# Kernel optimization log

Hardware: AMD Instinct MI355X
Metric: run time of the kernel (lower is better)

## Reference

```python
import jax, jax.numpy as jnp
import numpy as np

B, L, DIM, H = 2, 2048, 1024, 16
HD = DIM // H  # head dim = 64
MASK_SCALE = -10 * 6  # faithful to the original source: mask_expand *= -10 * 6


def setup_inputs() -> dict:
    key = jax.random.key(0)
    ks = jax.random.split(key, 8)
    s = 1.0 / np.sqrt(DIM)
    return {
        "x": jax.random.normal(ks[0], (B, L, DIM), jnp.float32),
        "attention_mask": jax.random.uniform(ks[1], (B, L, L), jnp.float32),
        "Wq": jax.random.normal(ks[2], (DIM, DIM), jnp.float32) * s,
        "bq": jnp.zeros((DIM,), jnp.float32),
        "Wk": jax.random.normal(ks[3], (DIM, DIM), jnp.float32) * s,
        "bk": jnp.zeros((DIM,), jnp.float32),
        "Wv": jax.random.normal(ks[4], (DIM, DIM), jnp.float32) * s,
        "bv": jnp.zeros((DIM,), jnp.float32),
    }


def _split_heads(t):
    # [B, L, DIM] -> [B, H, L, HD]
    return t.reshape(B, L, H, HD).transpose(0, 2, 1, 3)


def reference(x, attention_mask, Wq, bq, Wk, bk, Wv, bv):
    q = _split_heads(x @ Wq + bq)
    k = _split_heads(x @ Wk + bk)
    v = _split_heads(x @ Wv + bv)
    scale = float(HD) ** -0.5
    # full [B, H, L, L] score matrix, as in the original
    scores = jnp.einsum("bhqd,bhkd->bhqk", q, k) * scale
    scores = scores + attention_mask[:, None, :, :] * MASK_SCALE
    probs = jax.nn.softmax(scores, axis=-1)
    ctx = jnp.einsum("bhqk,bhkd->bhqd", probs, v)
    # merge heads back: [B, L, DIM]
    return ctx.transpose(0, 2, 1, 3).reshape(B, L, DIM)
```

## Files before the change

### kernel.cpp

```cpp
#include <hip/hip_runtime.h>

#define LL 2048
#define NHEADS 16
#define HDIM 64
#define QSCALE 0.18033688011112042f
#define MASKC1 -86.56170245333780f

typedef __attribute__((ext_vector_type(8))) __bf16 bf16x8;
typedef __attribute__((ext_vector_type(4))) float f32x4;
typedef __attribute__((ext_vector_type(16))) float f32x16;
typedef __attribute__((ext_vector_type(4))) int i32x4;

__device__ __forceinline__ unsigned short f2bf(float f) {
  unsigned int u = __builtin_bit_cast(unsigned int, f);
  u += 0x7fffu + ((u >> 16) & 1u);
  return (unsigned short)(u >> 16);
}

__device__ __forceinline__ bf16x8 ld_frag(const unsigned short* p) {
  return *reinterpret_cast<const bf16x8*>(p);
}

__device__ __forceinline__ void async_cp16(const unsigned short* g, unsigned short* l) {
  __builtin_amdgcn_global_load_lds(
      (const __attribute__((address_space(1))) unsigned int*)(unsigned long long)(g),
      (__attribute__((address_space(3))) unsigned int*)(unsigned int)(unsigned long long)(l),
      16, 0, 0);
}

__global__ __launch_bounds__(256) void prep_kernel(
    const float* __restrict__ x, const float* __restrict__ Wq, const float* __restrict__ Wk,
    const float* __restrict__ Wv, unsigned short* __restrict__ xb,
    unsigned short* __restrict__ WtAll) {
  __shared__ float t[64][65];
  int blk = blockIdx.x;
  if (blk < 4096) {
    int i = (blk * 256 + threadIdx.x) * 4;
    float4 v = *reinterpret_cast<const float4*>(x + i);
    ushort4 o;
    o.x = f2bf(v.x); o.y = f2bf(v.y); o.z = f2bf(v.z); o.w = f2bf(v.w);
    *reinterpret_cast<ushort4*>(xb + i) = o;
  } else {
    int idx = blk - 4096;
    int z = idx >> 8; idx &= 255;
    const float* W = (z == 0) ? Wq : (z == 1) ? Wk : Wv;
    unsigned short* dst = WtAll + (size_t)z * 1024 * 1024;
    int n0 = (idx & 15) * 64, k0 = (idx >> 4) * 64;
    int tx = threadIdx.x & 63, ty = threadIdx.x >> 6;
#pragma unroll
    for (int p = 0; p < 16; ++p) {
      int kr = p * 4 + ty;
      t[kr][tx] = W[(size_t)(k0 + kr) * 1024 + n0 + tx];
    }
    __syncthreads();
#pragma unroll
    for (int p = 0; p < 16; ++p) {
      int nr = p * 4 + ty;
      dst[(size_t)(n0 + nr) * 1024 + k0 + tx] = f2bf(t[tx][nr]);
    }
  }
}

__global__ __launch_bounds__(256) void em_prep_kernel(const float* __restrict__ mask,
                                                      unsigned short* __restrict__ em) {
  unsigned int t = blockIdx.x * 256 + threadIdx.x;
  int p = t & 15;
  int q = (t >> 4) & 2047;
  int kb = (t >> 15) & 31;
  int b = t >> 20;
  const float* src = mask + ((size_t)b * LL + q) * LL + kb * 64;
  ushort4 o;
  o.x = f2bf(__builtin_amdgcn_exp2f(src[2 * p]      * MASKC1));
  o.y = f2bf(__builtin_amdgcn_exp2f(src[32 + 2 * p] * MASKC1));
  o.z = f2bf(__builtin_amdgcn_exp2f(src[2 * p + 1]  * MASKC1));
  o.w = f2bf(__builtin_amdgcn_exp2f(src[33 + 2 * p] * MASKC1));
  *reinterpret_cast<ushort4*>(em + (((size_t)b * 32 + kb) * LL + q) * 64 + 4 * p) = o;
}

__global__ __launch_bounds__(256) void qkv_gemm_kernel(
    const unsigned short* __restrict__ xb, const unsigned short* __restrict__ WtAll,
    const float* __restrict__ bq, const float* __restrict__ bk, const float* __restrict__ bv,
    unsigned short* __restrict__ qkv) {
  const int z = blockIdx.z;
  const unsigned short* Wt = WtAll + (size_t)z * 1024 * 1024;
  const float* bias = (z == 0) ? bq : (z == 1) ? bk : bv;
  unsigned short* outb = qkv + (size_t)z * 4194304;

  __shared__ __align__(16) unsigned short smem[16384];
  unsigned short* As = smem;
  unsigned short* Bs = smem + 8192;

  const int tid = threadIdx.x;
  const int w = tid >> 6, lane = tid & 63, g = lane >> 4, cc = lane & 15;
  const int wm = w >> 1, wn = w & 1;
  const int m0 = blockIdx.y * 128, n0 = blockIdx.x * 128;
  const int srow = lane >> 3;
  const int gc = ((lane & 7) - srow) & 7;
  const unsigned short* ga = xb + (size_t)(m0 + w * 32 + srow) * 1024 + gc * 8;
  const unsigned short* gb = Wt + (size_t)(n0 + w * 32 + srow) * 1024 + gc * 8;
  unsigned short* la = As + w * 2048;
  unsigned short* lb = Bs + w * 2048;

  f32x4 acc[4][4];
#pragma unroll
  for (int i = 0; i < 4; ++i)
#pragma unroll
    for (int j = 0; j < 4; ++j) acc[i][j] = (f32x4)0.0f;

  for (int kk = 0; kk < 1024; kk += 64) {
    __syncthreads();
#pragma unroll
    for (int i = 0; i < 4; ++i) {
      async_cp16(ga + i * 8192 + kk, la + i * 512);
      async_cp16(gb + i * 8192 + kk, lb + i * 512);
    }
    __syncthreads();
    bf16x8 af[4][2], bfr[4][2];
#pragma unroll
    for (int mt = 0; mt < 4; ++mt)
#pragma unroll
      for (int ks = 0; ks < 2; ++ks)
        af[mt][ks] = ld_frag(&As[(wm * 64 + mt * 16 + cc) * 64 + ((4 * ks + g + cc) & 7) * 8]);
#pragma unroll
    for (int nt = 0; nt < 4; ++nt)
#pragma unroll
      for (int ks = 0; ks < 2; ++ks)
        bfr[nt][ks] = ld_frag(&Bs[(wn * 64 + nt * 16 + cc) * 64 + ((4 * ks + g + cc) & 7) * 8]);
#pragma unroll
    for (int mt = 0; mt < 4; ++mt)
#pragma unroll
      for (int nt = 0; nt < 4; ++nt)
#pragma unroll
        for (int ks = 0; ks < 2; ++ks)
          acc[mt][nt] = __builtin_amdgcn_mfma_f32_16x16x32_bf16(af[mt][ks], bfr[nt][ks],
                                                                acc[mt][nt], 0, 0, 0);
  }

  if (z != 2) {
    const float sc = (z == 0) ? QSCALE : 1.0f;
#pragma unroll
    for (int nt = 0; nt < 4; ++nt) {
      int n = n0 + wn * 64 + nt * 16 + cc;
      float bval = bias[n];
      int h = n >> 6, d = n & 63;
#pragma unroll
      for (int mt = 0; mt < 4; ++mt) {
#pragma unroll
        for (int r = 0; r < 4; ++r) {
          int m = m0 + wm * 64 + mt * 16 + g * 4 + r;
          int b = m >> 11, l = m & 2047;
          outb[(((size_t)(b * NHEADS + h) * LL) + l) * HDIM + d] =
              f2bf((acc[mt][nt][r] + bval) * sc);
        }
      }
    }
  } else {
    __syncthreads();
#pragma unroll
    for (int nt = 0; nt < 4; ++nt) {
      int nr = wn * 64 + nt * 16 + cc;
      float bval = bias[n0 + nr];
#pragma unroll
      for (int mt = 0; mt < 4; ++mt)
#pragma unroll
        for (int r = 0; r < 4; ++r)
          smem[nr * 128 + wm * 64 + 32 * (mt & 1) + 8 * g + 2 * r + (mt >> 1)] =
              f2bf(acc[mt][nt][r] + bval);
    }
    __syncthreads();
    int row = tid >> 1, half = tid & 1;
    int n = n0 + row, hh = n >> 6, dd = n & 63;
    int bb = m0 >> 11;
    int tI = ((m0 & 2047) >> 6) + half;
    unsigned short* dst =
        outb + (size_t)(bb * NHEADS + hh) * (LL * HDIM) + (size_t)tI * 4096 + dd * 64;
#pragma unroll
    for (int i = 0; i < 8; ++i)
      *reinterpret_cast<uint4*>(dst + i * 8) =
          *reinterpret_cast<const uint4*>(&smem[row * 128 + half * 64 + i * 8]);
  }
}

__global__ __launch_bounds__(128, 2) void flash_kernel(
    const unsigned short* __restrict__ Qb, const unsigned short* __restrict__ Kb,
    const unsigned short* __restrict__ Vt, const unsigned short* __restrict__ Em,
    float* __restrict__ out) {
  const int bh = blockIdx.y, b = bh >> 4, h = bh & 15;
  const int q0 = blockIdx.x * 64;
  const int tid = threadIdx.x, w = tid >> 6, lane = tid & 63;
  const int cl = lane & 31, hf = lane >> 5;
  const size_t bhoff = (size_t)bh * (LL * HDIM);

  __shared__ __align__(16) unsigned short Ks[2][64 * 64];
  __shared__ __align__(16) unsigned short Vs[2][64 * 64];
  __shared__ __align__(16) unsigned short Ps[2][32 * 64];
  unsigned short* myP = Ps[w];

  bf16x8 aq[4];
  {
    const unsigned short* qp = Qb + bhoff + (size_t)(q0 + w * 32 + cl) * HDIM + hf * 8;
#pragma unroll
    for (int ks = 0; ks < 4; ++ks) aq[ks] = ld_frag(qp + ks * 16);
  }

  const int srow = lane >> 3;
  const int gcs = ((lane & 7) - srow) & 7;
  const unsigned short* kgp = Kb + bhoff + (size_t)(w * 32 + srow) * 64 + gcs * 8;
  const unsigned short* vgp = Vt + bhoff + (size_t)(w * 32 + srow) * 64 + gcs * 8;

  i32x4 onesi = {0x3F803F80, 0x3F803F80, 0x3F803F80, 0x3F803F80};
  bf16x8 vones = __builtin_bit_cast(bf16x8, onesi);

  f32x16 oacc0 = (f32x16)0.0f, oacc1 = (f32x16)0.0f, liacc = (f32x16)0.0f;

  const unsigned short* ebase =
      Em + (((size_t)b * 32) * LL + (q0 + w * 32 + 4 * hf)) * 64 + 2 * cl;

#pragma unroll
  for (int i = 0; i < 4; ++i) {
    async_cp16(kgp + i * 512, Ks[0] + w * 2048 + i * 512);
    async_cp16(vgp + i * 512, Vs[0] + w * 2048 + i * 512);
  }
  unsigned int emv[16];
#pragma unroll
  for (int r = 0; r < 16; ++r)
    emv[r] = *reinterpret_cast<const unsigned int*>(
        ebase + (size_t)((r & 3) + 8 * (r >> 2)) * 64);

#pragma unroll 2
  for (int kt = 0; kt < 32; ++kt) {
    const int buf = kt & 1;
    __syncthreads();
    if (kt + 1 < 32) {
      const int nb = buf ^ 1;
      const unsigned short* ksrc = kgp + (size_t)(kt + 1) * 4096;
      const unsigned short* vsrc = vgp + (size_t)(kt + 1) * 4096;
#pragma unroll
      for (int i = 0; i < 4; ++i) {
        async_cp16(ksrc + i * 512, Ks[nb] + w * 2048 + i * 512);
        async_cp16(vsrc + i * 512, Vs[nb] + w * 2048 + i * 512);
      }
    }
    const int ktn = (kt + 1 < 32) ? kt + 1 : 31;
    unsigned int emn[16];
#pragma unroll
    for (int r = 0; r < 16; ++r)
      emn[r] = *reinterpret_cast<const unsigned int*>(
          ebase + (size_t)ktn * 131072 + (size_t)((r & 3) + 8 * (r >> 2)) * 64);

    bf16x8 bk[2][4];
#pragma unroll
    for (int t = 0; t < 2; ++t)
#pragma unroll
      for (int ks = 0; ks < 4; ++ks) {
        int row = t * 32 + cl;
        bk[t][ks] = ld_frag(&Ks[buf][row * 64 + (((2 * ks + hf + row) & 7) << 3)]);
      }
    f32x16 s0 = (f32x16)0.0f, s1 = (f32x16)0.0f;
#pragma unroll
    for (int ks = 0; ks < 4; ++ks) {
      s0 = __builtin_amdgcn_mfma_f32_32x32x16_bf16(aq[ks], bk[0][ks], s0, 0, 0, 0);
      s1 = __builtin_amdgcn_mfma_f32_32x32x16_bf16(aq[ks], bk[1][ks], s1, 0, 0, 0);
    }

#pragma unroll
    for (int r = 0; r < 16; ++r) {
      unsigned int eu = emv[r];
      float e0 = __builtin_bit_cast(float, eu << 16);
      float e1 = __builtin_bit_cast(float, eu & 0xffff0000u);
      float p0 = __builtin_amdgcn_exp2f(s0[r]) * e0;
      float p1 = __builtin_amdgcn_exp2f(s1[r]) * e1;
      unsigned int u = __builtin_amdgcn_perm(__builtin_bit_cast(unsigned int, p1),
                                             __builtin_bit_cast(unsigned int, p0),
                                             0x07060302u);
      int R = (r & 3) + 8 * (r >> 2) + 4 * hf;
      *reinterpret_cast<unsigned int*>(
          &myP[R * 64 + ((((cl >> 2) + R) & 7) << 3) + 2 * (cl & 3)]) = u;
    }
    asm volatile("" ::: "memory");

    bf16x8 ap[4];
#pragma unroll
    for (int ks = 0; ks < 4; ++ks)
      ap[ks] = ld_frag(&myP[cl * 64 + (((2 * ks + hf + cl) & 7) << 3)]);
    bf16x8 bv[2][4];
#pragma unroll
    for (int t = 0; t < 2; ++t)
#pragma unroll
      for (int ks = 0; ks < 4; ++ks) {
        int row = t * 32 + cl;
        bv[t][ks] = ld_frag(&Vs[buf][row * 64 + (((2 * ks + hf + row) & 7) << 3)]);
      }
#pragma unroll
    for (int ks = 0; ks < 4; ++ks) {
      oacc0 = __builtin_amdgcn_mfma_f32_32x32x16_bf16(ap[ks], bv[0][ks], oacc0, 0, 0, 0);
      oacc1 = __builtin_amdgcn_mfma_f32_32x32x16_bf16(ap[ks], bv[1][ks], oacc1, 0, 0, 0);
      liacc = __builtin_amdgcn_mfma_f32_32x32x16_bf16(ap[ks], vones, liacc, 0, 0, 0);
    }
#pragma unroll
    for (int r = 0; r < 16; ++r) emv[r] = emn[r];
  }

#pragma unroll
  for (int r = 0; r < 16; ++r) {
    float inv = 1.0f / liacc[r];
    int q = q0 + w * 32 + (r & 3) + 8 * (r >> 2) + 4 * hf;
    float* op = out + ((size_t)b * LL + q) * 1024 + h * 64 + cl;
    op[0]  = oacc0[r] * inv;
    op[32] = oacc1[r] * inv;
  }
}

extern "C" void kernel_launch(void* const* d_in, const int* in_sizes, int n_in,
                              void* d_out, int out_size, void* d_ws, size_t ws_size,
                              hipStream_t stream) {
  const float* x    = (const float*)d_in[0];
  const float* mask = (const float*)d_in[1];
  const float* Wq   = (const float*)d_in[2];
  const float* bq   = (const float*)d_in[3];
  const float* Wk   = (const float*)d_in[4];
  const float* bk   = (const float*)d_in[5];
  const float* Wv   = (const float*)d_in[6];
  const float* bv   = (const float*)d_in[7];
  float* out = (float*)d_out;
  (void)in_sizes; (void)n_in; (void)out_size; (void)ws_size;

  char* ws = (char*)d_ws;
  unsigned short* qkv = (unsigned short*)(ws);
  unsigned short* xb  = (unsigned short*)(ws + (24u << 20));
  unsigned short* Wt  = (unsigned short*)(ws + (32u << 20));
  unsigned short* em  = (unsigned short*)(ws + (24u << 20));

  prep_kernel<<<dim3(4864), dim3(256), 0, stream>>>(x, Wq, Wk, Wv, xb, Wt);
  qkv_gemm_kernel<<<dim3(8, 32, 3), dim3(256), 0, stream>>>(xb, Wt, bq, bk, bv, qkv);
  em_prep_kernel<<<dim3(8192), dim3(256), 0, stream>>>(mask, em);
  flash_kernel<<<dim3(32, 32), dim3(128), 0, stream>>>(qkv, qkv + 4194304, qkv + 8388608,
                                                       em, out);
}
```

Before: 218.3 us.

## Split key tiles across warps in flash kernel with larger query blocks

The flash kernel moves to 512-thread blocks covering 128 queries. Each of 8 warps handles 32 query rows and one half of each 64-key tile, and the two key-half partial outputs and row sums are combined through shared memory at the end. The mask-exponent prep kernel becomes a shared-memory transpose so the flash kernel reads mask values in a layout that matches the new per-warp split. The V transpose layout in the GEMM epilogue is changed to match. This is meant to raise wave occupancy and share K/V tiles across more query rows, at the cost of a final cross-warp reduction and more sync per tile.

```diff
diff --git a/kernel.cpp b/kernel.cpp
--- a/kernel.cpp
+++ b/kernel.cpp
@@ -63,18 +63,24 @@
 
 __global__ __launch_bounds__(256) void em_prep_kernel(const float* __restrict__ mask,
                                                       unsigned short* __restrict__ em) {
-  unsigned int t = blockIdx.x * 256 + threadIdx.x;
-  int p = t & 15;
-  int q = (t >> 4) & 2047;
-  int kb = (t >> 15) & 31;
-  int b = t >> 20;
-  const float* src = mask + ((size_t)b * LL + q) * LL + kb * 64;
-  ushort4 o;
-  o.x = f2bf(__builtin_amdgcn_exp2f(src[2 * p]      * MASKC1));
-  o.y = f2bf(__builtin_amdgcn_exp2f(src[32 + 2 * p] * MASKC1));
-  o.z = f2bf(__builtin_amdgcn_exp2f(src[2 * p + 1]  * MASKC1));
-  o.w = f2bf(__builtin_amdgcn_exp2f(src[33 + 2 * p] * MASKC1));
-  *reinterpret_cast<ushort4*>(em + (((size_t)b * 32 + kb) * LL + q) * 64 + 4 * p) = o;
+  __shared__ float t[64][65];
+  int blk = blockIdx.x;
+  int qt = blk & 31, kt = (blk >> 5) & 31, b = blk >> 10;
+  int q0 = qt * 64;
+  int tx = threadIdx.x & 63, ty = threadIdx.x >> 6;
+#pragma unroll
+  for (int p = 0; p < 16; ++p) {
+    int qr = p * 4 + ty;
+    t[qr][tx] = mask[((size_t)b * LL + q0 + qr) * LL + kt * 64 + tx];
+  }
+  __syncthreads();
+#pragma unroll
+  for (int p = 0; p < 16; ++p) {
+    int c64 = p * 4 + ty;
+    int kh = c64 >> 5, c = c64 & 31;
+    em[((((size_t)b * 32 + kt) * 2 + kh) * 32 + c) * LL + q0 + tx] =
+        f2bf(__builtin_amdgcn_exp2f(t[tx][c64] * MASKC1));
+  }
 }
 
 __global__ __launch_bounds__(256) void qkv_gemm_kernel(
@@ -164,8 +170,7 @@
       for (int mt = 0; mt < 4; ++mt)
 #pragma unroll
         for (int r = 0; r < 4; ++r)
-          smem[nr * 128 + wm * 64 + 32 * (mt & 1) + 8 * g + 2 * r + (mt >> 1)] =
-              f2bf(acc[mt][nt][r] + bval);
+          smem[nr * 128 + wm * 64 + mt * 16 + g * 4 + r] = f2bf(acc[mt][nt][r] + bval);
     }
     __syncthreads();
     int row = tid >> 1, half = tid & 1;
@@ -181,32 +186,33 @@
   }
 }
 
-__global__ __launch_bounds__(128, 2) void flash_kernel(
+__global__ __launch_bounds__(512, 4) void flash_kernel(
     const unsigned short* __restrict__ Qb, const unsigned short* __restrict__ Kb,
     const unsigned short* __restrict__ Vt, const unsigned short* __restrict__ Em,
     float* __restrict__ out) {
   const int bh = blockIdx.y, b = bh >> 4, h = bh & 15;
-  const int q0 = blockIdx.x * 64;
+  const int q0 = blockIdx.x * 128;
   const int tid = threadIdx.x, w = tid >> 6, lane = tid & 63;
   const int cl = lane & 31, hf = lane >> 5;
+  const int rg = w & 3, kh = w >> 2;
   const size_t bhoff = (size_t)bh * (LL * HDIM);
 
-  __shared__ __align__(16) unsigned short Ks[2][64 * 64];
-  __shared__ __align__(16) unsigned short Vs[2][64 * 64];
-  __shared__ __align__(16) unsigned short Ps[2][32 * 64];
-  unsigned short* myP = Ps[w];
+  __shared__ __align__(16) unsigned short smem[32768];
+  unsigned short* Kbuf = smem;
+  unsigned short* Vbuf = smem + 8192;
+  unsigned short* myP  = smem + 16384 + w * 2048;
 
   bf16x8 aq[4];
   {
-    const unsigned short* qp = Qb + bhoff + (size_t)(q0 + w * 32 + cl) * HDIM + hf * 8;
+    const unsigned short* qp = Qb + bhoff + (size_t)(q0 + rg * 32 + cl) * HDIM + hf * 8;
 #pragma unroll
     for (int ks = 0; ks < 4; ++ks) aq[ks] = ld_frag(qp + ks * 16);
   }
 
   const int srow = lane >> 3;
   const int gcs = ((lane & 7) - srow) & 7;
-  const unsigned short* kgp = Kb + bhoff + (size_t)(w * 32 + srow) * 64 + gcs * 8;
-  const unsigned short* vgp = Vt + bhoff + (size_t)(w * 32 + srow) * 64 + gcs * 8;
+  const unsigned short* kgp = Kb + bhoff + (size_t)(w * 8 + srow) * 64 + gcs * 8;
+  const unsigned short* vgp = Vt + bhoff + (size_t)(w * 8 + srow) * 64 + gcs * 8;
 
   i32x4 onesi = {0x3F803F80, 0x3F803F80, 0x3F803F80, 0x3F803F80};
   bf16x8 vones = __builtin_bit_cast(bf16x8, onesi);
@@ -214,18 +220,14 @@
   f32x16 oacc0 = (f32x16)0.0f, oacc1 = (f32x16)0.0f, liacc = (f32x16)0.0f;
 
   const unsigned short* ebase =
-      Em + (((size_t)b * 32) * LL + (q0 + w * 32 + 4 * hf)) * 64 + 2 * cl;
-
-#pragma unroll
-  for (int i = 0; i < 4; ++i) {
-    async_cp16(kgp + i * 512, Ks[0] + w * 2048 + i * 512);
-    async_cp16(vgp + i * 512, Vs[0] + w * 2048 + i * 512);
-  }
-  unsigned int emv[16];
-#pragma unroll
-  for (int r = 0; r < 16; ++r)
-    emv[r] = *reinterpret_cast<const unsigned int*>(
-        ebase + (size_t)((r & 3) + 8 * (r >> 2)) * 64);
+      Em + ((((size_t)b * 32) * 2 + kh) * 32 + cl) * LL + (q0 + rg * 32 + 4 * hf);
+
+  async_cp16(kgp, Kbuf + w * 512);
+  async_cp16(vgp, Vbuf + w * 512);
+  uint2 emv[4];
+#pragma unroll
+  for (int m = 0; m < 4; ++m)
+    emv[m] = *reinterpret_cast<const uint2*>(ebase + m * 8);
 
 #pragma unroll 2
   for (int kt = 0; kt < 32; ++kt) {
@@ -233,81 +235,91 @@
     __syncthreads();
     if (kt + 1 < 32) {
       const int nb = buf ^ 1;
-      const unsigned short* ksrc = kgp + (size_t)(kt + 1) * 4096;
-      const unsigned short* vsrc = vgp + (size_t)(kt + 1) * 4096;
-#pragma unroll
-      for (int i = 0; i < 4; ++i) {
-        async_cp16(ksrc + i * 512, Ks[nb] + w * 2048 + i * 512);
-        async_cp16(vsrc + i * 512, Vs[nb] + w * 2048 + i * 512);
+      async_cp16(kgp + (size_t)(kt + 1) * 4096, Kbuf + nb * 4096 + w * 512);
+      async_cp16(vgp + (size_t)(kt + 1) * 4096, Vbuf + nb * 4096 + w * 512);
+    }
+    const int ktn = (kt + 1 < 32) ? kt + 1 : 31;
+    uint2 emn[4];
+#pragma unroll
+    for (int m = 0; m < 4; ++m)
+      emn[m] = *reinterpret_cast<const uint2*>(ebase + (size_t)ktn * 131072 + m * 8);
+
+    bf16x8 bkf[4];
+#pragma unroll
+    for (int ks = 0; ks < 4; ++ks) {
+      int row = kh * 32 + cl;
+      bkf[ks] = ld_frag(&Kbuf[buf * 4096 + row * 64 + ((2 * ks + hf + row) & 7) * 8]);
+    }
+    f32x16 sacc = (f32x16)0.0f;
+#pragma unroll
+    for (int ks = 0; ks < 4; ++ks)
+      sacc = __builtin_amdgcn_mfma_f32_32x32x16_bf16(aq[ks], bkf[ks], sacc, 0, 0, 0);
+
+#pragma unroll
+    for (int m = 0; m < 4; ++m) {
+      unsigned int ex = emv[m].x, ey = emv[m].y;
+      float ef[4];
+      ef[0] = __builtin_bit_cast(float, ex << 16);
+      ef[1] = __builtin_bit_cast(float, ex & 0xffff0000u);
+      ef[2] = __builtin_bit_cast(float, ey << 16);
+      ef[3] = __builtin_bit_cast(float, ey & 0xffff0000u);
+#pragma unroll
+      for (int j = 0; j < 4; ++j) {
+        int r = 4 * m + j;
+        float p = __builtin_amdgcn_exp2f(sacc[r]) * ef[j];
+        int qh = j + 8 * m + 4 * hf;
+        myP[qh * 64 + (((cl >> 3) + qh) & 7) * 8 + (cl & 7)] =
+            (unsigned short)(__builtin_bit_cast(unsigned int, p) >> 16);
       }
     }
-    const int ktn = (kt + 1 < 32) ? kt + 1 : 31;
-    unsigned int emn[16];
-#pragma unroll
-    for (int r = 0; r < 16; ++r)
-      emn[r] = *reinterpret_cast<const unsigned int*>(
-          ebase + (size_t)ktn * 131072 + (size_t)((r & 3) + 8 * (r >> 2)) * 64);
-
-    bf16x8 bk[2][4];
+    asm volatile("" ::: "memory");
+
+    bf16x8 ap[2];
+#pragma unroll
+    for (int ks = 0; ks < 2; ++ks)
+      ap[ks] = ld_frag(&myP[cl * 64 + ((2 * ks + hf + cl) & 7) * 8]);
+    bf16x8 bvf[2][2];
 #pragma unroll
     for (int t = 0; t < 2; ++t)
 #pragma unroll
-      for (int ks = 0; ks < 4; ++ks) {
+      for (int ks = 0; ks < 2; ++ks) {
         int row = t * 32 + cl;
-        bk[t][ks] = ld_frag(&Ks[buf][row * 64 + (((2 * ks + hf + row) & 7) << 3)]);
+        bvf[t][ks] = ld_frag(
+            &Vbuf[buf * 4096 + row * 64 + ((4 * kh + 2 * ks + hf + row) & 7) * 8]);
       }
-    f32x16 s0 = (f32x16)0.0f, s1 = (f32x16)0.0f;
-#pragma unroll
-    for (int ks = 0; ks < 4; ++ks) {
-      s0 = __builtin_amdgcn_mfma_f32_32x32x16_bf16(aq[ks], bk[0][ks], s0, 0, 0, 0);
-      s1 = __builtin_amdgcn_mfma_f32_32x32x16_bf16(aq[ks], bk[1][ks], s1, 0, 0, 0);
-    }
-
+#pragma unroll
+    for (int ks = 0; ks < 2; ++ks) {
+      oacc0 = __builtin_amdgcn_mfma_f32_32x32x16_bf16(ap[ks], bvf[0][ks], oacc0, 0, 0, 0);
+      oacc1 = __builtin_amdgcn_mfma_f32_32x32x16_bf16(ap[ks], bvf[1][ks], oacc1, 0, 0, 0);
+      liacc = __builtin_amdgcn_mfma_f32_32x32x16_bf16(ap[ks], vones, liacc, 0, 0, 0);
+    }
+#pragma unroll
+    for (int m = 0; m < 4; ++m) emv[m] = emn[m];
+  }
+
+  __syncthreads();
+  float* Om = reinterpret_cast<float*>(smem);
+  if (kh == 1) {
 #pragma unroll
     for (int r = 0; r < 16; ++r) {
-      unsigned int eu = emv[r];
-      float e0 = __builtin_bit_cast(float, eu << 16);
-      float e1 = __builtin_bit_cast(float, eu & 0xffff0000u);
-      float p0 = __builtin_amdgcn_exp2f(s0[r]) * e0;
-      float p1 = __builtin_amdgcn_exp2f(s1[r]) * e1;
-      unsigned int u = __builtin_amdgcn_perm(__builtin_bit_cast(unsigned int, p1),
-                                             __builtin_bit_cast(unsigned int, p0),
-                                             0x07060302u);
       int R = (r & 3) + 8 * (r >> 2) + 4 * hf;
-      *reinterpret_cast<unsigned int*>(
-          &myP[R * 64 + ((((cl >> 2) + R) & 7) << 3) + 2 * (cl & 3)]) = u;
-    }
-    asm volatile("" ::: "memory");
-
-    bf16x8 ap[4];
-#pragma unroll
-    for (int ks = 0; ks < 4; ++ks)
-      ap[ks] = ld_frag(&myP[cl * 64 + (((2 * ks + hf + cl) & 7) << 3)]);
-    bf16x8 bv[2][4];
-#pragma unroll
-    for (int t = 0; t < 2; ++t)
-#pragma unroll
-      for (int ks = 0; ks < 4; ++ks) {
-        int row = t * 32 + cl;
-        bv[t][ks] = ld_frag(&Vs[buf][row * 64 + (((2 * ks + hf + row) & 7) << 3)]);
-      }
-#pragma unroll
-    for (int ks = 0; ks < 4; ++ks) {
-      oacc0 = __builtin_amdgcn_mfma_f32_32x32x16_bf16(ap[ks], bv[0][ks], oacc0, 0, 0, 0);
-      oacc1 = __builtin_amdgcn_mfma_f32_32x32x16_bf16(ap[ks], bv[1][ks], oacc1, 0, 0, 0);
-      liacc = __builtin_amdgcn_mfma_f32_32x32x16_bf16(ap[ks], vones, liacc, 0, 0, 0);
-    }
-#pragma unroll
-    for (int r = 0; r < 16; ++r) emv[r] = emn[r];
-  }
-
-#pragma unroll
-  for (int r = 0; r < 16; ++r) {
-    float inv = 1.0f / liacc[r];
-    int q = q0 + w * 32 + (r & 3) + 8 * (r >> 2) + 4 * hf;
-    float* op = out + ((size_t)b * LL + q) * 1024 + h * 64 + cl;
-    op[0]  = oacc0[r] * inv;
-    op[32] = oacc1[r] * inv;
+      Om[rg * 2080 + R * 64 + cl]      = oacc0[r];
+      Om[rg * 2080 + R * 64 + 32 + cl] = oacc1[r];
+      if (cl == 0) Om[rg * 2080 + 2048 + R] = liacc[r];
+    }
+  }
+  __syncthreads();
+  if (kh == 0) {
+#pragma unroll
+    for (int r = 0; r < 16; ++r) {
+      int R = (r & 3) + 8 * (r >> 2) + 4 * hf;
+      float lsum = liacc[r] + Om[rg * 2080 + 2048 + R];
+      float inv = 1.0f / lsum;
+      int q = q0 + rg * 32 + R;
+      float* op = out + ((size_t)b * LL + q) * 1024 + h * 64 + cl;
+      op[0]  = (oacc0[r] + Om[rg * 2080 + R * 64 + cl])      * inv;
+      op[32] = (oacc1[r] + Om[rg * 2080 + R * 64 + 32 + cl]) * inv;
+    }
   }
 }
 
@@ -333,7 +345,7 @@
 
   prep_kernel<<<dim3(4864), dim3(256), 0, stream>>>(x, Wq, Wk, Wv, xb, Wt);
   qkv_gemm_kernel<<<dim3(8, 32, 3), dim3(256), 0, stream>>>(xb, Wt, bq, bk, bv, qkv);
-  em_prep_kernel<<<dim3(8192), dim3(256), 0, stream>>>(mask, em);
-  flash_kernel<<<dim3(32, 32), dim3(128), 0, stream>>>(qkv, qkv + 4194304, qkv + 8388608,
+  em_prep_kernel<<<dim3(2048), dim3(256), 0, stream>>>(mask, em);
+  flash_kernel<<<dim3(16, 32), dim3(512), 0, stream>>>(qkv, qkv + 4194304, qkv + 8388608,
                                                        em, out);
 }
```

Measured after the change: 257.6 us. 18.0% more time.
